# Optimization experiments

Measured on AMD Instinct MI355X. Metric: run time of the kernel, lower is better.

## Reference

```python
import jax, jax.numpy as jnp
import numpy as np

# ---- Cl(3,0) geometric-algebra Cayley table (8 blades: 1,e1,e2,e3,e12,e13,e23,e123) ----
# T[k, i, j] = sign s.t. blade_i * blade_j = sign * blade_k (exactly 8 (i,j) pairs per k).

def _build_cayley():
    masks = [0b000, 0b001, 0b010, 0b100, 0b011, 0b101, 0b110, 0b111]
    T = np.zeros((8, 8, 8), np.float32)
    for i, a in enumerate(masks):
        for j, b in enumerate(masks):
            k = masks.index(a ^ b)
            aa, s = a >> 1, 0
            while aa:
                s += bin(aa & b).count('1')
                aa >>= 1
            T[k, i, j] = -1.0 if (s & 1) else 1.0
    return jnp.asarray(T)

CAYLEY = _build_cayley()
LN_EPS = 1e-5  # torch LayerNorm default


def _layer_norm(x, w, b):
    mu = jnp.mean(x, axis=-1, keepdims=True)
    var = jnp.var(x, axis=-1, keepdims=True)
    return (x - mu) * jax.lax.rsqrt(var + LN_EPS) * w + b


def _expert_forward(x_e, p_in, p_out, iw, gg, w_gate, w_up, w_down, lnw, lnb, out_w, out_b):
    # x_e: (C, D); p_in: (D, ED); per-round params indexed [r]
    C = x_e.shape[0]
    DB = lnw.shape[-1]
    mv = (x_e @ p_in).reshape(C, 8, DB)  # (C, n_blades, d_blade)
    n_rounds = iw.shape[0]
    for r in range(n_rounds):
        w = jax.nn.sigmoid(iw[r]).reshape(8, 8)          # interaction weights w[i,j]
        gate = jax.nn.sigmoid(gg[r])                      # scalar geo gate
        # geo[n,k,d] = sum_{i,j} sign[k,i,j] * w[i,j] * mv[n,i,d] * mv[n,j,d]
        geo = jnp.einsum('kij,ij,nid,njd->nkd', CAYLEY, w, mv, mv)
        mixed = gate * geo + (1.0 - gate) * mv
        flat = _layer_norm(mixed, lnw[r], lnb[r])         # LN over d_blade
        h = jax.nn.silu(flat @ w_gate[r]) * (flat @ w_up[r])  # SwiGLU
        mv = mv + h @ w_down[r]                           # residual
    out = mv.reshape(C, -1) @ p_out                       # (C, D)
    return _layer_norm(out, out_w, out_b)


def setup_inputs() -> dict:
    key = jax.random.key(0)
    ks = jax.random.split(key, 8)
    E, D, NB, DB, R, F = 16, 1024, 8, 64, 2, 256
    ED = NB * DB
    N = 32768
    C = N // E
    std = 0.02
    return {
        'x_sorted': jax.random.normal(ks[0], (N, D), jnp.float32),
        'proj_in': jax.random.normal(ks[1], (E, D, ED), jnp.float32) * std,
        'proj_out': jax.random.normal(ks[2], (E, ED, D), jnp.float32) * std,
        'interaction_weights': jnp.ones((E, R, 64), jnp.float32) * 0.1,
        'geo_gates': jnp.ones((E, R), jnp.float32) * 0.5,
        'ffn_gate': jax.random.normal(ks[3], (E, R, DB, F), jnp.float32) * std,
        'ffn_up': jax.random.normal(ks[4], (E, R, DB, F), jnp.float32) * std,
        'ffn_down': jax.random.normal(ks[5], (E, R, F, DB), jnp.float32) * std,
        'ffn_ln_w': jnp.ones((E, R, DB), jnp.float32),
        'ffn_ln_b': jnp.zeros((E, R, DB), jnp.float32),
        'out_ln_w': jnp.ones((D,), jnp.float32),
        'out_ln_b': jnp.zeros((D,), jnp.float32),
        'expert_offsets': jnp.arange(E, dtype=jnp.int32) * C,
        'expert_counts': jnp.full((E,), C, dtype=jnp.int32),
    }


def reference(x_sorted, proj_in, proj_out, interaction_weights, geo_gates,
              ffn_gate, ffn_up, ffn_down, ffn_ln_w, ffn_ln_b,
              out_ln_w, out_ln_b, expert_offsets, expert_counts):
    E = proj_in.shape[0]
    N, D = x_sorted.shape
    C = N // E  # balanced routing: equal tokens per expert (static shapes)
    idx = expert_offsets[:, None].astype(jnp.int32) + jnp.arange(C, dtype=jnp.int32)[None, :]
    x_b = x_sorted[idx]  # (E, C, D) gather of sorted tokens per expert
    y_b = jax.vmap(_expert_forward,
                   in_axes=(0, 0, 0, 0, 0, 0, 0, 0, 0, 0, None, None))(
        x_b, proj_in, proj_out, interaction_weights, geo_gates,
        ffn_gate, ffn_up, ffn_down, ffn_ln_w, ffn_ln_b, out_ln_w, out_ln_b)
    y = jnp.zeros_like(x_sorted).at[idx.reshape(-1)].set(y_b.reshape(-1, D))
    return y
```

## Files before the change

### kernel.cpp

```cpp
#include <hip/hip_runtime.h>

#define DEV __device__ __forceinline__

typedef __attribute__((ext_vector_type(4))) float f32x4;
typedef __attribute__((ext_vector_type(2))) float f32x2;
typedef __attribute__((ext_vector_type(8))) short bf16x8;


DEV unsigned short f2bf(float f) {
  union { float f; unsigned u; } v; v.f = f;
  unsigned r = v.u + 0x7fffu + ((v.u >> 16) & 1u);
  return (unsigned short)(r >> 16);
}

DEV unsigned pk2bf(float lo, float hi) {
  unsigned r;
  asm("v_cvt_pk_bf16_f32 %0, %1, %2" : "=v"(r) : "v"(lo), "v"(hi));
  return r;
}
DEV unsigned short f2bf1(float v) { return (unsigned short)pk2bf(v, v); }

DEV float bf2f(unsigned short b) {
  union { unsigned u; float f; } v; v.u = ((unsigned)b) << 16; return v.f;
}

DEV float frcp(float x) { return __builtin_amdgcn_rcpf(x); }

DEV void sbar() { asm volatile("s_barrier" ::: "memory"); }
DEV void wait_lgkm0() { asm volatile("s_waitcnt lgkmcnt(0)" ::: "memory"); }
DEV void wait_vm0() { asm volatile("s_waitcnt vmcnt(0)" ::: "memory"); }

DEV void async16(const unsigned short* g, unsigned short* l) {
  __builtin_amdgcn_global_load_lds(
      (__attribute__((address_space(1))) const unsigned int*)g,
      (__attribute__((address_space(3))) unsigned int*)l, 16, 0, 0);
}

DEV long tiled_off(long n, int k, int K) {
  return (n >> 3) * (8L * K) + (long)(((k >> 3) * 64) + ((int)(n & 7)) * 8 + (k & 7));
}

DEV bf16x8 ld_frag(const char* s, int row, int hi) {
  return *(const bf16x8*)(s + ((row >> 3) * 512 + hi * 128 + (row & 7) * 16));
}

__host__ __device__ constexpr int km_(int i) { return i==0?0:i==1?1:i==2?2:i==3?4:i==4?3:i==5?5:i==6?6:7; }
__host__ __device__ constexpr int pc_(int x) { int c = 0; while (x) { c += x & 1; x >>= 1; } return c; }
__host__ __device__ constexpr int KIDX(int i, int j) { return km_(km_(i) ^ km_(j)); }
__host__ __device__ constexpr int CSGN(int i, int j) {
  int a = km_(i), b = km_(j), aa = a >> 1, s = 0;
  while (aa) { s += pc_(aa & b); aa >>= 1; }
  return (s & 1) ? -1 : 1;
}
__host__ __device__ constexpr int PIDX(int i, int j) {
  return 8 * i - (i * (i - 1)) / 2 + (j - i);
}

__global__ __launch_bounds__(64) void geoprep_k(const float* __restrict__ iw,
                                                const float* __restrict__ gg,
                                                float* __restrict__ wcomb) {
  int er = threadIdx.x;
  if (er >= 32) return;
  const float* w = iw + er * 64;
  float gate = frcp(1.f + __expf(-gg[er]));
  float* c = wcomb + er * 40;
  int p = 0;
  for (int i = 0; i < 8; ++i)
    for (int j = i; j < 8; ++j) {
      float v = (float)CSGN(i, j) * frcp(1.f + __expf(-w[i * 8 + j]));
      if (j > i) v += (float)CSGN(j, i) * frcp(1.f + __expf(-w[j * 8 + i]));
      c[p++] = gate * v;
    }
  c[36] = 1.f - gate;
}

template<int TI>
__global__ __launch_bounds__(256) void transpose_k(const float* __restrict__ in,
                                                   unsigned short* __restrict__ out,
                                                   int Rr, int Cc) {
  __shared__ unsigned short tile[32][33];
  const float* ib = in + (long)blockIdx.z * Rr * Cc;
  unsigned short* ob = out + (long)blockIdx.z * Rr * Cc;
  int r0 = blockIdx.y * 32, c0 = blockIdx.x * 32;
  int tr = threadIdx.x >> 5, tc = threadIdx.x & 31;
#pragma unroll
  for (int i = 0; i < 4; ++i) {
    int r = tr + i * 8;
    tile[r][tc] = f2bf(ib[(long)(r0 + r) * Cc + c0 + tc]);
  }
  __syncthreads();
#pragma unroll
  for (int i = 0; i < 4; ++i) {
    int c = tr + i * 8;
    int row = c0 + c;
    int k = r0 + tc;
    if (TI == 0) ob[(long)row * Rr + k] = tile[tc][c];
    else ob[(long)row * Rr + (k ^ ((row & 7) << 3))] = tile[tc][c];
  }
}

__global__ __launch_bounds__(256) void trans_big_k(const float* __restrict__ in,
                                                   unsigned short* __restrict__ out,
                                                   int Rr, int Cc) {
  __shared__ float t[64][64];
  const float* ib = in + (long)blockIdx.z * Rr * Cc;
  unsigned short* ob = out + (long)blockIdx.z * (long)Rr * Cc;
  int k0 = blockIdx.y * 64, n0 = blockIdx.x * 64;
  int tid = threadIdx.x;
#pragma unroll
  for (int p = 0; p < 4; ++p) {
    int idx = p * 256 + tid;
    int kr = idx >> 4, nc = (idx & 15) * 4;
    *(float4*)&t[kr][nc] = *(const float4*)(ib + (long)(k0 + kr) * Cc + n0 + nc);
  }
  __syncthreads();
#pragma unroll
  for (int p = 0; p < 2; ++p) {
    int idx = p * 256 + tid;
    int n = idx & 63, kc = idx >> 6;
    float v[8];
#pragma unroll
    for (int u = 0; u < 8; ++u) v[u] = t[kc * 8 + u][n];
    uint4 o;
    o.x = pk2bf(v[0], v[1]); o.y = pk2bf(v[2], v[3]);
    o.z = pk2bf(v[4], v[5]); o.w = pk2bf(v[6], v[7]);
    *(uint4*)(ob + tiled_off(n0 + n, k0 + kc * 8, Rr)) = o;
  }
}

__global__ __launch_bounds__(512, 1) void gemm_in_k(const float* __restrict__ X,
                                                    const unsigned short* __restrict__ Bw,
                                                    unsigned short* __restrict__ MvB,
                                                    const int* __restrict__ offs) {
  extern __shared__ char smem[];
  int bid = blockIdx.x;
  int wg = (bid & 7) * 32 + (bid >> 3);
  int e = wg >> 4, rem = wg & 15, bm = rem >> 1, bn = rem & 1;
  int tid = threadIdx.x, wid = tid >> 6, lane = tid & 63;
  int wm = (wid >> 2) * 128, wn = (wid & 3) * 64;
  int ri = lane & 15, hi = lane >> 4;
  long rowbase = (long)offs[e] + bm * 256;
  long bw = (long)e * 64 + bn * 32;

  auto STGB = [&](int p) {
    int t = p >> 1, s = p & 1, b = t & 1;
    char* dst = smem + b * 65536 + 32768 + s * 16384;
#pragma unroll
    for (int i = 0; i < 2; ++i) {
      int d = i * 512 + tid;
      async16(Bw + (bw + (d >> 5)) * 8192 +
                  (long)((t * 8 + s * 4 + ((d >> 3) & 3)) * 64 + (d & 7) * 8),
              (unsigned short*)(dst + d * 16));
    }
  };
  auto A_LOAD = [&](int p, float4 ar[2][2]) {
    int t = p >> 1, s = p & 1;
#pragma unroll
    for (int i = 0; i < 2; ++i) {
      int d = i * 512 + tid;
      const float* src = X + (rowbase + ((d >> 5) * 8 + (d & 7))) * 1024 +
                         t * 64 + s * 32 + ((d >> 3) & 3) * 8;
      ar[i][0] = *(const float4*)src;
      ar[i][1] = *(const float4*)(src + 4);
    }
  };
  auto A_WRITE = [&](int p, float4 ar[2][2]) {
    int t = p >> 1, s = p & 1, b = t & 1;
    char* dst = smem + b * 65536 + s * 16384;
#pragma unroll
    for (int i = 0; i < 2; ++i) {
      int d = i * 512 + tid;
      uint4 o;
      o.x = pk2bf(ar[i][0].x, ar[i][0].y);
      o.y = pk2bf(ar[i][0].z, ar[i][0].w);
      o.z = pk2bf(ar[i][1].x, ar[i][1].y);
      o.w = pk2bf(ar[i][1].z, ar[i][1].w);
      *(uint4*)(dst + d * 16) = o;
    }
  };

  f32x4 acc[8][4];
#pragma unroll
  for (int i = 0; i < 8; ++i)
#pragma unroll
    for (int j = 0; j < 4; ++j) acc[i][j] = (f32x4){0.f, 0.f, 0.f, 0.f};

  float4 ar[2][2];
  A_LOAD(0, ar); STGB(0); STGB(1);
  A_WRITE(0, ar);
  A_LOAD(1, ar);
  A_WRITE(1, ar);
  wait_lgkm0();

#pragma unroll 2
  for (int p = 0; p < 32; ++p) {
    int t = p >> 1, s = p & 1, c = t & 1;
    if (p < 30) { A_LOAD(p + 2, ar); STGB(p + 2); }
    if (p < 30) asm volatile("s_waitcnt vmcnt(8)" ::: "memory");
    else if (p == 30) asm volatile("s_waitcnt vmcnt(2)" ::: "memory");
    else asm volatile("s_waitcnt vmcnt(0)" ::: "memory");
    sbar();
    const char* cA = smem + c * 65536 + s * 16384;
    const char* cB = smem + c * 65536 + 32768 + s * 16384;
    bf16x8 a[8], b[4];
#pragma unroll
    for (int i = 0; i < 8; ++i) a[i] = ld_frag(cA, wm + i * 16 + ri, hi);
#pragma unroll
    for (int j = 0; j < 4; ++j) b[j] = ld_frag(cB, wn + j * 16 + ri, hi);
    __builtin_amdgcn_s_setprio(1);
#pragma unroll
    for (int i = 0; i < 8; ++i)
#pragma unroll
      for (int j = 0; j < 4; ++j)
        acc[i][j] = __builtin_amdgcn_mfma_f32_16x16x32_bf16(a[i], b[j], acc[i][j], 0, 0, 0);
    __builtin_amdgcn_s_setprio(0);
    if (p < 30) A_WRITE(p + 2, ar);
    wait_lgkm0();
  }

  unsigned short* Cb = MvB + ((long)e * 2048 + (long)bm * 256) * 512 + bn * 256;
#pragma unroll
  for (int i = 0; i < 8; ++i)
#pragma unroll
    for (int j = 0; j < 4; ++j)
#pragma unroll
      for (int rr = 0; rr < 4; ++rr)
        Cb[(long)(wm + i * 16 + hi * 4 + rr) * 512 + wn + j * 16 + ri] =
            f2bf1(acc[i][j][rr]);
}

__global__ __launch_bounds__(256, 3) void rounds_k(
    const unsigned short* __restrict__ MvB, const unsigned short* __restrict__ WgT,
    const unsigned short* __restrict__ WuT, const unsigned short* __restrict__ WdT,
    const float* __restrict__ wcomb, const float* __restrict__ lnw,
    const float* __restrict__ lnb, unsigned short* __restrict__ Mvb) {
  extern __shared__ char smem[];
  int tid = threadIdx.x, wid = tid >> 6, lane = tid & 63;
  char* sFH = smem + wid * 4096;
  char* sMv = smem + 16384 + wid * 4096;
  char* sW  = smem + 32768;

  int bid = blockIdx.x;
  int wg = (bid & 7) * 256 + (bid >> 3);
  int e = wg >> 7, bx = wg & 127;

  int t4 = lane >> 4, q = lane & 15;
  int ri = lane & 15, hi = lane >> 4;
  int sw = (ri & 7) << 4;

  auto STAGE = [&](int i8) {
    long base = (long)(e * 2 + (i8 >> 3)) * 16384 + (i8 & 7) * 2048;
    char* dst = sW + (i8 & 1) * 8192;
    async16(WgT + base + tid * 8, (unsigned short*)(dst + tid * 16));
    async16(WuT + base + tid * 8, (unsigned short*)(dst + 4096 + tid * 16));
  };
  STAGE(0);

#pragma unroll 1
  for (int r = 0; r < 2; ++r) {
    int er = e * 2 + r;
    const unsigned short* wd = WdT + (long)er * 16384;

    f32x4 mv[8];
    if (r == 0) {
      long base = ((long)e * 2048 + bx * 16 + wid * 4 + t4) * 512 + 4 * q;
      uint2 uv[8];
#pragma unroll
      for (int i = 0; i < 8; ++i)
        uv[i] = *(const uint2*)(MvB + base + i * 64);
#pragma unroll
      for (int i = 0; i < 8; ++i) {
        *(uint2*)(sMv + t4 * 1024 + i * 128 + ((8 * q) ^ (i << 4))) = uv[i];
        mv[i] = (f32x4){bf2f((unsigned short)(uv[i].x & 0xffff)),
                        bf2f((unsigned short)(uv[i].x >> 16)),
                        bf2f((unsigned short)(uv[i].y & 0xffff)),
                        bf2f((unsigned short)(uv[i].y >> 16))};
      }
    } else {
#pragma unroll
      for (int i = 0; i < 8; ++i) {
        uint2 uv = *(const uint2*)(sMv + t4 * 1024 + i * 128 + ((8 * q) ^ (i << 4)));
        mv[i] = (f32x4){bf2f((unsigned short)(uv.x & 0xffff)),
                        bf2f((unsigned short)(uv.x >> 16)),
                        bf2f((unsigned short)(uv.y & 0xffff)),
                        bf2f((unsigned short)(uv.y >> 16))};
      }
    }

    {
      const float* C = wcomb + er * 40;
      f32x4 g[8];
#pragma unroll
      for (int k = 0; k < 8; ++k) g[k] = (f32x4){0.f, 0.f, 0.f, 0.f};
#pragma unroll
      for (int i = 0; i < 8; ++i)
#pragma unroll
        for (int j = i; j < 8; ++j) {
          float cc = C[PIDX(i, j)];
          const int k = KIDX(i, j);
          g[k] += cc * (mv[i] * mv[j]);
        }
      float omg = C[36];
#pragma unroll
      for (int k = 0; k < 8; ++k) g[k] = omg * mv[k] + g[k];
      float4 lw = *(const float4*)(lnw + (long)er * 64 + 4 * q);
      float4 lb = *(const float4*)(lnb + (long)er * 64 + 4 * q);
      f32x4 lwv = (f32x4){lw.x, lw.y, lw.z, lw.w};
      f32x4 lbv = (f32x4){lb.x, lb.y, lb.z, lb.w};
#pragma unroll
      for (int half = 0; half < 2; ++half) {
        f32x2 red[4];
#pragma unroll
        for (int k = 0; k < 4; ++k) {
          f32x4 m = g[half * 4 + k];
          red[k].x = (m.x + m.y) + (m.z + m.w);
          red[k].y = fmaf(m.x, m.x, m.y * m.y) + fmaf(m.z, m.z, m.w * m.w);
        }
#pragma unroll
        for (int off = 8; off >= 1; off >>= 1)
#pragma unroll
          for (int t = 0; t < 4; ++t) {
            f32x2 o;
            o.x = __shfl_xor(red[t].x, off);
            o.y = __shfl_xor(red[t].y, off);
            red[t] += o;
          }
#pragma unroll
        for (int k = 0; k < 4; ++k) {
          int kk = half * 4 + k;
          float mean = red[k].x * (1.f / 64.f);
          float var = red[k].y * (1.f / 64.f) - mean * mean;
          float rs = rsqrtf(var + 1e-5f);
          f32x4 nv = (g[kk] - mean) * rs;
          f32x4 ov = nv * lwv + lbv;
          uint2 pv;
          pv.x = pk2bf(ov.x, ov.y);
          pv.y = pk2bf(ov.z, ov.w);
          int row = t4 * 8 + kk;
          *(uint2*)(sFH + row * 128 + ((8 * q) ^ (kk << 4))) = pv;
        }
      }
    }
    wait_lgkm0();

    bf16x8 bfr[2][2];
#pragma unroll
    for (int tt = 0; tt < 2; ++tt)
#pragma unroll
      for (int kt = 0; kt < 2; ++kt)
        bfr[tt][kt] = *(const bf16x8*)(sFH + (tt * 16 + ri) * 128 + ((kt * 64 + hi * 16) ^ sw));

    f32x4 acc2[4][2];
#pragma unroll
    for (int j = 0; j < 4; ++j)
#pragma unroll
      for (int tt = 0; tt < 2; ++tt) acc2[j][tt] = (f32x4){0.f, 0.f, 0.f, 0.f};

#pragma unroll 1
    for (int q8 = 0; q8 < 8; ++q8) {
      int i8 = r * 8 + q8;
      wait_vm0();
      sbar();
      if (i8 < 15) STAGE(i8 + 1);

      bf16x8 wdf[4];
#pragma unroll
      for (int j = 0; j < 4; ++j)
        wdf[j] = *(const bf16x8*)(wd + (j * 16 + ri) * 256 + q8 * 32 + hi * 8);

      const char* bufW = sW + (i8 & 1) * 8192;

#pragma unroll
      for (int ftl = 0; ftl < 2; ++ftl) {
        const char* bg = bufW + (ftl * 16 + ri) * 128;
        const char* bu = bg + 4096;
        bf16x8 wg0 = *(const bf16x8*)(bg + ((hi * 16) ^ sw));
        bf16x8 wg1 = *(const bf16x8*)(bg + ((64 + hi * 16) ^ sw));
        bf16x8 wu0 = *(const bf16x8*)(bu + ((hi * 16) ^ sw));
        bf16x8 wu1 = *(const bf16x8*)(bu + ((64 + hi * 16) ^ sw));
        f32x4 ag[2], au[2];
#pragma unroll
        for (int tt = 0; tt < 2; ++tt) {
          ag[tt] = (f32x4){0.f, 0.f, 0.f, 0.f};
          au[tt] = (f32x4){0.f, 0.f, 0.f, 0.f};
        }
        __builtin_amdgcn_s_setprio(1);
#pragma unroll
        for (int tt = 0; tt < 2; ++tt) {
          ag[tt] = __builtin_amdgcn_mfma_f32_16x16x32_bf16(wg0, bfr[tt][0], ag[tt], 0, 0, 0);
          au[tt] = __builtin_amdgcn_mfma_f32_16x16x32_bf16(wu0, bfr[tt][0], au[tt], 0, 0, 0);
          ag[tt] = __builtin_amdgcn_mfma_f32_16x16x32_bf16(wg1, bfr[tt][1], ag[tt], 0, 0, 0);
          au[tt] = __builtin_amdgcn_mfma_f32_16x16x32_bf16(wu1, bfr[tt][1], au[tt], 0, 0, 0);
        }
        __builtin_amdgcn_s_setprio(0);
#pragma unroll
        for (int tt = 0; tt < 2; ++tt) {
          float hh[4];
#pragma unroll
          for (int rr = 0; rr < 4; ++rr) {
            float gv = ag[tt][rr], uu = au[tt][rr];
            hh[rr] = gv * uu * frcp(1.f + __expf(-gv));
          }
          uint2 hwv;
          hwv.x = pk2bf(hh[0], hh[1]);
          hwv.y = pk2bf(hh[2], hh[3]);
          *(uint2*)(sFH + (tt * 16 + ri) * 128 + ((ftl * 32 + hi * 8) ^ sw)) = hwv;
        }
      }
      wait_lgkm0();

      bf16x8 hk0 = *(const bf16x8*)(sFH + ri * 128 + ((hi * 16) ^ sw));
      bf16x8 hk1 = *(const bf16x8*)(sFH + (16 + ri) * 128 + ((hi * 16) ^ sw));
      __builtin_amdgcn_s_setprio(1);
#pragma unroll
      for (int j = 0; j < 4; ++j)
        acc2[j][0] = __builtin_amdgcn_mfma_f32_16x16x32_bf16(wdf[j], hk0, acc2[j][0], 0, 0, 0);
#pragma unroll
      for (int j = 0; j < 4; ++j)
        acc2[j][1] = __builtin_amdgcn_mfma_f32_16x16x32_bf16(wdf[j], hk1, acc2[j][1], 0, 0, 0);
      __builtin_amdgcn_s_setprio(0);
    }

    {
#pragma unroll
      for (int tt = 0; tt < 2; ++tt) {
        int tl = tt * 2 + (ri >> 3);
        int kb = ri & 7;
#pragma unroll
        for (int j = 0; j < 4; ++j)
#pragma unroll
          for (int u = 0; u < 2; ++u) {
            int off = (j * 32 + hi * 8 + 4 * u) ^ sw;
            unsigned* p = (unsigned*)(sMv + tl * 1024 + kb * 128 + off);
            unsigned old = *p;
            float v0 = bf2f((unsigned short)(old & 0xffff)) + acc2[j][tt][2 * u];
            float v1 = bf2f((unsigned short)(old >> 16)) + acc2[j][tt][2 * u + 1];
            *p = pk2bf(v0, v1);
          }
      }
    }
    wait_lgkm0();

    if (r == 1) {
      int tt = lane >> 4;
      int idx = lane & 15;
      int bl = idx >> 1;
      int c2 = idx & 1;
      const char* src = sMv + tt * 1024 + bl * 128;
      long row = (long)e * 2048 + bx * 16 + wid * 4 + tt;
      unsigned short* dst = Mvb + row * 512 + bl * 64 + c2 * 32;
#pragma unroll
      for (int h = 0; h < 4; ++h) {
        uint4 v = *(const uint4*)(src + ((c2 * 64 + h * 16) ^ (bl << 4)));
        *(uint4*)(dst + h * 8) = v;
      }
    }
  }
}

__global__ __launch_bounds__(512, 2) void gemm_out_ln_k(
    const unsigned short* __restrict__ Mvb, const unsigned short* __restrict__ Pw,
    float* __restrict__ Out, const float* __restrict__ ow, const float* __restrict__ ob,
    const int* __restrict__ offs) {
  extern __shared__ char smem[];
  int bid = blockIdx.x;
  int wg = (bid & 7) * 64 + (bid >> 3);
  int e = wg >> 5, mb = wg & 31;
  int tid = threadIdx.x, wid = tid >> 6, lane = tid & 63;
  int ri = lane & 15, hi = lane >> 4;
  long bbase = (long)e * 524288;
  long arow0 = (long)e * 2048 + (long)mb * 64;

  auto STAGE = [&](int buf, int kt) {
#pragma unroll
    for (int i = 0; i < 8; ++i) {
      int q = i * 512 + tid;
      int w = q >> 5, c = (q >> 3) & 3, rr = q & 7;
      async16(Pw + bbase + (long)w * 4096 + (kt * 4 + c) * 64 + rr * 8,
              (unsigned short*)(smem + buf * 65536 + q * 16));
    }
    if (tid < 256) {
      int q = tid;
      int w = q >> 5, c = (q >> 3) & 3, rr = q & 7;
      async16(Mvb + (arow0 + w * 8 + rr) * 512 + kt * 32 + c * 8,
              (unsigned short*)(smem + 131072 + buf * 4096 + q * 16));
    }
  };

  f32x4 acc[4][8];
#pragma unroll
  for (int i = 0; i < 4; ++i)
#pragma unroll
    for (int j = 0; j < 8; ++j) acc[i][j] = (f32x4){0.f, 0.f, 0.f, 0.f};

  STAGE(0, 0);
  for (int kt = 0; kt < 16; ++kt) {
    int cur = kt & 1;
    if (kt < 15) {
      STAGE(cur ^ 1, kt + 1);
      asm volatile("s_waitcnt vmcnt(8)" ::: "memory");
    } else {
      asm volatile("s_waitcnt vmcnt(0)" ::: "memory");
    }
    sbar();
    const char* cB = smem + cur * 65536;
    const char* cA = smem + 131072 + cur * 4096;
    bf16x8 a[4], b[8];
#pragma unroll
    for (int i = 0; i < 4; ++i) a[i] = ld_frag(cA, i * 16 + ri, hi);
#pragma unroll
    for (int j = 0; j < 8; ++j) b[j] = ld_frag(cB, wid * 128 + j * 16 + ri, hi);
    __builtin_amdgcn_s_setprio(1);
#pragma unroll
    for (int i = 0; i < 4; ++i)
#pragma unroll
      for (int j = 0; j < 8; ++j)
        acc[i][j] = __builtin_amdgcn_mfma_f32_16x16x32_bf16(a[i], b[j], acc[i][j], 0, 0, 0);
    __builtin_amdgcn_s_setprio(0);
    sbar();
  }

  float* rsum = (float*)(smem + 139264);
  float* rsq  = (float*)(smem + 141312);
  float* mexp = (float*)(smem + 143360);
  float* rstd = (float*)(smem + 143616);
  int hi4 = hi * 4;
#pragma unroll
  for (int i = 0; i < 4; ++i)
#pragma unroll
    for (int rr = 0; rr < 4; ++rr) {
      float s = 0.f, qv = 0.f;
#pragma unroll
      for (int j = 0; j < 8; ++j) { float v = acc[i][j][rr]; s += v; qv += v * v; }
#pragma unroll
      for (int off = 1; off < 16; off <<= 1) {
        s += __shfl_xor(s, off);
        qv += __shfl_xor(qv, off);
      }
      if (ri == 0) {
        int row = i * 16 + hi4 + rr;
        rsum[row * 8 + wid] = s;
        rsq[row * 8 + wid] = qv;
      }
    }
  __syncthreads();
  if (tid < 64) {
    float S = 0.f, Q = 0.f;
#pragma unroll
    for (int w = 0; w < 8; ++w) { S += rsum[tid * 8 + w]; Q += rsq[tid * 8 + w]; }
    float mean = S * (1.f / 1024.f);
    float var = Q * (1.f / 1024.f) - mean * mean;
    mexp[tid] = mean;
    rstd[tid] = rsqrtf(var + 1e-5f);
  }
  __syncthreads();
  long r0 = (long)offs[e] + (long)mb * 64;
  float owv[8], obv[8];
#pragma unroll
  for (int j = 0; j < 8; ++j) {
    int col = wid * 128 + j * 16 + ri;
    owv[j] = ow[col];
    obv[j] = ob[col];
  }
#pragma unroll
  for (int i = 0; i < 4; ++i)
#pragma unroll
    for (int rr = 0; rr < 4; ++rr) {
      int row = i * 16 + hi4 + rr;
      float mu = mexp[row], rs = rstd[row];
#pragma unroll
      for (int j = 0; j < 8; ++j) {
        int col = wid * 128 + j * 16 + ri;
        Out[(r0 + row) * 1024 + col] = (acc[i][j][rr] - mu) * rs * owv[j] + obv[j];
      }
    }
}

extern "C" void kernel_launch(void* const* d_in, const int* in_sizes, int n_in,
                              void* d_out, int out_size, void* d_ws, size_t ws_size,
                              hipStream_t stream) {
  const float* x    = (const float*)d_in[0];
  const float* pin  = (const float*)d_in[1];
  const float* pout = (const float*)d_in[2];
  const float* iw   = (const float*)d_in[3];
  const float* gg   = (const float*)d_in[4];
  const float* fg   = (const float*)d_in[5];
  const float* fu   = (const float*)d_in[6];
  const float* fd   = (const float*)d_in[7];
  const float* lnw  = (const float*)d_in[8];
  const float* lnb  = (const float*)d_in[9];
  const float* ow   = (const float*)d_in[10];
  const float* ob   = (const float*)d_in[11];
  const int* offs   = (const int*)d_in[12];

  char* ws = (char*)d_ws;
  unsigned short* mvB  = (unsigned short*)(ws + 0L);
  unsigned short* mvb  = (unsigned short*)(ws + 33554432L);
  unsigned short* pinT = (unsigned short*)(ws + 67108864L);
  unsigned short* poutT= (unsigned short*)(ws + 83886080L);
  unsigned short* wgT  = (unsigned short*)(ws + 100663296L);
  unsigned short* wuT  = (unsigned short*)(ws + 102760448L);
  unsigned short* wdT  = (unsigned short*)(ws + 104857600L);
  float* wcomb         = (float*)(ws + 106954752L);

  trans_big_k<<<dim3(8, 16, 16), dim3(256), 0, stream>>>(pin, pinT, 1024, 512);
  trans_big_k<<<dim3(16, 8, 16), dim3(256), 0, stream>>>(pout, poutT, 512, 1024);
  transpose_k<1><<<dim3(8, 2, 32), dim3(256), 0, stream>>>(fg, wgT, 64, 256);
  transpose_k<1><<<dim3(8, 2, 32), dim3(256), 0, stream>>>(fu, wuT, 64, 256);
  transpose_k<0><<<dim3(2, 8, 32), dim3(256), 0, stream>>>(fd, wdT, 256, 64);
  geoprep_k<<<dim3(1), dim3(64), 0, stream>>>(iw, gg, wcomb);

  gemm_in_k<<<dim3(256), dim3(512), 131072, stream>>>(x, pinT, mvB, offs);

  rounds_k<<<dim3(2048), dim3(256), 49152, stream>>>(
      mvB, wgT, wuT, wdT, wcomb, lnw, lnb, mvb);

  gemm_out_ln_k<<<dim3(512), dim3(512), 143872, stream>>>(
      mvb, poutT, (float*)d_out, ow, ob, offs);
}
```

Measured before the change: 274.4 us.

## Double tokens per wave in rounds kernel to amortize weight fragment loads

```diff
diff --git a/kernel.cpp b/kernel.cpp
--- a/kernel.cpp
+++ b/kernel.cpp
@@ -229,22 +229,22 @@
             f2bf1(acc[i][j][rr]);
 }
 
-__global__ __launch_bounds__(256, 3) void rounds_k(
+__global__ __launch_bounds__(256, 2) void rounds_k(
     const unsigned short* __restrict__ MvB, const unsigned short* __restrict__ WgT,
     const unsigned short* __restrict__ WuT, const unsigned short* __restrict__ WdT,
     const float* __restrict__ wcomb, const float* __restrict__ lnw,
     const float* __restrict__ lnb, unsigned short* __restrict__ Mvb) {
   extern __shared__ char smem[];
   int tid = threadIdx.x, wid = tid >> 6, lane = tid & 63;
-  char* sFH = smem + wid * 4096;
-  char* sMv = smem + 16384 + wid * 4096;
-  char* sW  = smem + 32768;
+  char* sFH = smem + wid * 8192;
+  char* sMv = smem + 32768 + wid * 8192;
+  char* sW  = smem + 65536;
 
   int bid = blockIdx.x;
-  int wg = (bid & 7) * 256 + (bid >> 3);
-  int e = wg >> 7, bx = wg & 127;
-
-  int t4 = lane >> 4, q = lane & 15;
+  int wg = (bid & 7) * 128 + (bid >> 3);
+  int e = wg >> 6, bx = wg & 63;
+
+  int t8 = lane >> 3, q = lane & 7;
   int ri = lane & 15, hi = lane >> 4;
   int sw = (ri & 7) << 4;
 
@@ -261,63 +261,81 @@
     int er = e * 2 + r;
     const unsigned short* wd = WdT + (long)er * 16384;
 
-    f32x4 mv[8];
+    f32x4 mv[2][8];
     if (r == 0) {
-      long base = ((long)e * 2048 + bx * 16 + wid * 4 + t4) * 512 + 4 * q;
-      uint2 uv[8];
+      long base = ((long)e * 2048 + bx * 32 + wid * 8 + t8) * 512 + 8 * q;
+      uint4 uv[8];
 #pragma unroll
       for (int i = 0; i < 8; ++i)
-        uv[i] = *(const uint2*)(MvB + base + i * 64);
+        uv[i] = *(const uint4*)(MvB + base + i * 64);
 #pragma unroll
       for (int i = 0; i < 8; ++i) {
-        *(uint2*)(sMv + t4 * 1024 + i * 128 + ((8 * q) ^ (i << 4))) = uv[i];
-        mv[i] = (f32x4){bf2f((unsigned short)(uv[i].x & 0xffff)),
-                        bf2f((unsigned short)(uv[i].x >> 16)),
-                        bf2f((unsigned short)(uv[i].y & 0xffff)),
-                        bf2f((unsigned short)(uv[i].y >> 16))};
+        *(uint4*)(sMv + t8 * 1024 + i * 128 + ((16 * q) ^ (i << 4))) = uv[i];
+        mv[0][i] = (f32x4){bf2f((unsigned short)(uv[i].x & 0xffff)),
+                           bf2f((unsigned short)(uv[i].x >> 16)),
+                           bf2f((unsigned short)(uv[i].y & 0xffff)),
+                           bf2f((unsigned short)(uv[i].y >> 16))};
+        mv[1][i] = (f32x4){bf2f((unsigned short)(uv[i].z & 0xffff)),
+                           bf2f((unsigned short)(uv[i].z >> 16)),
+                           bf2f((unsigned short)(uv[i].w & 0xffff)),
+                           bf2f((unsigned short)(uv[i].w >> 16))};
       }
     } else {
 #pragma unroll
       for (int i = 0; i < 8; ++i) {
-        uint2 uv = *(const uint2*)(sMv + t4 * 1024 + i * 128 + ((8 * q) ^ (i << 4)));
-        mv[i] = (f32x4){bf2f((unsigned short)(uv.x & 0xffff)),
-                        bf2f((unsigned short)(uv.x >> 16)),
-                        bf2f((unsigned short)(uv.y & 0xffff)),
-                        bf2f((unsigned short)(uv.y >> 16))};
+        uint4 uv = *(const uint4*)(sMv + t8 * 1024 + i * 128 + ((16 * q) ^ (i << 4)));
+        mv[0][i] = (f32x4){bf2f((unsigned short)(uv.x & 0xffff)),
+                           bf2f((unsigned short)(uv.x >> 16)),
+                           bf2f((unsigned short)(uv.y & 0xffff)),
+                           bf2f((unsigned short)(uv.y >> 16))};
+        mv[1][i] = (f32x4){bf2f((unsigned short)(uv.z & 0xffff)),
+                           bf2f((unsigned short)(uv.z >> 16)),
+                           bf2f((unsigned short)(uv.w & 0xffff)),
+                           bf2f((unsigned short)(uv.w >> 16))};
       }
     }
 
     {
       const float* C = wcomb + er * 40;
-      f32x4 g[8];
-#pragma unroll
-      for (int k = 0; k < 8; ++k) g[k] = (f32x4){0.f, 0.f, 0.f, 0.f};
+      f32x4 g[2][8];
+#pragma unroll
+      for (int hf = 0; hf < 2; ++hf)
+#pragma unroll
+        for (int k = 0; k < 8; ++k) g[hf][k] = (f32x4){0.f, 0.f, 0.f, 0.f};
 #pragma unroll
       for (int i = 0; i < 8; ++i)
 #pragma unroll
         for (int j = i; j < 8; ++j) {
           float cc = C[PIDX(i, j)];
           const int k = KIDX(i, j);
-          g[k] += cc * (mv[i] * mv[j]);
+          g[0][k] += cc * (mv[0][i] * mv[0][j]);
+          g[1][k] += cc * (mv[1][i] * mv[1][j]);
         }
       float omg = C[36];
 #pragma unroll
-      for (int k = 0; k < 8; ++k) g[k] = omg * mv[k] + g[k];
-      float4 lw = *(const float4*)(lnw + (long)er * 64 + 4 * q);
-      float4 lb = *(const float4*)(lnb + (long)er * 64 + 4 * q);
-      f32x4 lwv = (f32x4){lw.x, lw.y, lw.z, lw.w};
-      f32x4 lbv = (f32x4){lb.x, lb.y, lb.z, lb.w};
-#pragma unroll
-      for (int half = 0; half < 2; ++half) {
+      for (int hf = 0; hf < 2; ++hf)
+#pragma unroll
+        for (int k = 0; k < 8; ++k) g[hf][k] = omg * mv[hf][k] + g[hf][k];
+      float4 lwa = *(const float4*)(lnw + (long)er * 64 + 8 * q);
+      float4 lwb = *(const float4*)(lnw + (long)er * 64 + 8 * q + 4);
+      float4 lba = *(const float4*)(lnb + (long)er * 64 + 8 * q);
+      float4 lbb = *(const float4*)(lnb + (long)er * 64 + 8 * q + 4);
+      f32x4 lwvA = (f32x4){lwa.x, lwa.y, lwa.z, lwa.w};
+      f32x4 lwvB = (f32x4){lwb.x, lwb.y, lwb.z, lwb.w};
+      f32x4 lbvA = (f32x4){lba.x, lba.y, lba.z, lba.w};
+      f32x4 lbvB = (f32x4){lbb.x, lbb.y, lbb.z, lbb.w};
+#pragma unroll
+      for (int bh = 0; bh < 2; ++bh) {
         f32x2 red[4];
 #pragma unroll
         for (int k = 0; k < 4; ++k) {
-          f32x4 m = g[half * 4 + k];
-          red[k].x = (m.x + m.y) + (m.z + m.w);
-          red[k].y = fmaf(m.x, m.x, m.y * m.y) + fmaf(m.z, m.z, m.w * m.w);
+          f32x4 a = g[0][bh * 4 + k], b = g[1][bh * 4 + k];
+          red[k].x = ((a.x + a.y) + (a.z + a.w)) + ((b.x + b.y) + (b.z + b.w));
+          red[k].y = (fmaf(a.x, a.x, a.y * a.y) + fmaf(a.z, a.z, a.w * a.w)) +
+                     (fmaf(b.x, b.x, b.y * b.y) + fmaf(b.z, b.z, b.w * b.w));
         }
 #pragma unroll
-        for (int off = 8; off >= 1; off >>= 1)
+        for (int off = 4; off >= 1; off >>= 1)
 #pragma unroll
           for (int t = 0; t < 4; ++t) {
             f32x2 o;
@@ -327,34 +345,36 @@
           }
 #pragma unroll
         for (int k = 0; k < 4; ++k) {
-          int kk = half * 4 + k;
+          int kk = bh * 4 + k;
           float mean = red[k].x * (1.f / 64.f);
           float var = red[k].y * (1.f / 64.f) - mean * mean;
           float rs = rsqrtf(var + 1e-5f);
-          f32x4 nv = (g[kk] - mean) * rs;
-          f32x4 ov = nv * lwv + lbv;
-          uint2 pv;
-          pv.x = pk2bf(ov.x, ov.y);
-          pv.y = pk2bf(ov.z, ov.w);
-          int row = t4 * 8 + kk;
-          *(uint2*)(sFH + row * 128 + ((8 * q) ^ (kk << 4))) = pv;
+          f32x4 ovA = ((g[0][kk] - mean) * rs) * lwvA + lbvA;
+          f32x4 ovB = ((g[1][kk] - mean) * rs) * lwvB + lbvB;
+          uint4 pv;
+          pv.x = pk2bf(ovA.x, ovA.y);
+          pv.y = pk2bf(ovA.z, ovA.w);
+          pv.z = pk2bf(ovB.x, ovB.y);
+          pv.w = pk2bf(ovB.z, ovB.w);
+          int row = t8 * 8 + kk;
+          *(uint4*)(sFH + row * 128 + ((16 * q) ^ (kk << 4))) = pv;
         }
       }
     }
     wait_lgkm0();
 
-    bf16x8 bfr[2][2];
-#pragma unroll
-    for (int tt = 0; tt < 2; ++tt)
+    bf16x8 bfr[4][2];
+#pragma unroll
+    for (int tt = 0; tt < 4; ++tt)
 #pragma unroll
       for (int kt = 0; kt < 2; ++kt)
         bfr[tt][kt] = *(const bf16x8*)(sFH + (tt * 16 + ri) * 128 + ((kt * 64 + hi * 16) ^ sw));
 
-    f32x4 acc2[4][2];
+    f32x4 acc2[4][4];
 #pragma unroll
     for (int j = 0; j < 4; ++j)
 #pragma unroll
-      for (int tt = 0; tt < 2; ++tt) acc2[j][tt] = (f32x4){0.f, 0.f, 0.f, 0.f};
+      for (int tt = 0; tt < 4; ++tt) acc2[j][tt] = (f32x4){0.f, 0.f, 0.f, 0.f};
 
 #pragma unroll 1
     for (int q8 = 0; q8 < 8; ++q8) {
@@ -378,15 +398,15 @@
         bf16x8 wg1 = *(const bf16x8*)(bg + ((64 + hi * 16) ^ sw));
         bf16x8 wu0 = *(const bf16x8*)(bu + ((hi * 16) ^ sw));
         bf16x8 wu1 = *(const bf16x8*)(bu + ((64 + hi * 16) ^ sw));
-        f32x4 ag[2], au[2];
-#pragma unroll
-        for (int tt = 0; tt < 2; ++tt) {
+        f32x4 ag[4], au[4];
+#pragma unroll
+        for (int tt = 0; tt < 4; ++tt) {
           ag[tt] = (f32x4){0.f, 0.f, 0.f, 0.f};
           au[tt] = (f32x4){0.f, 0.f, 0.f, 0.f};
         }
         __builtin_amdgcn_s_setprio(1);
 #pragma unroll
-        for (int tt = 0; tt < 2; ++tt) {
+        for (int tt = 0; tt < 4; ++tt) {
           ag[tt] = __builtin_amdgcn_mfma_f32_16x16x32_bf16(wg0, bfr[tt][0], ag[tt], 0, 0, 0);
           au[tt] = __builtin_amdgcn_mfma_f32_16x16x32_bf16(wu0, bfr[tt][0], au[tt], 0, 0, 0);
           ag[tt] = __builtin_amdgcn_mfma_f32_16x16x32_bf16(wg1, bfr[tt][1], ag[tt], 0, 0, 0);
@@ -394,7 +414,7 @@
         }
         __builtin_amdgcn_s_setprio(0);
 #pragma unroll
-        for (int tt = 0; tt < 2; ++tt) {
+        for (int tt = 0; tt < 4; ++tt) {
           float hh[4];
 #pragma unroll
           for (int rr = 0; rr < 4; ++rr) {
@@ -409,21 +429,22 @@
       }
       wait_lgkm0();
 
-      bf16x8 hk0 = *(const bf16x8*)(sFH + ri * 128 + ((hi * 16) ^ sw));
-      bf16x8 hk1 = *(const bf16x8*)(sFH + (16 + ri) * 128 + ((hi * 16) ^ sw));
+      bf16x8 hk[4];
+#pragma unroll
+      for (int tt = 0; tt < 4; ++tt)
+        hk[tt] = *(const bf16x8*)(sFH + (tt * 16 + ri) * 128 + ((hi * 16) ^ sw));
       __builtin_amdgcn_s_setprio(1);
 #pragma unroll
       for (int j = 0; j < 4; ++j)
-        acc2[j][0] = __builtin_amdgcn_mfma_f32_16x16x32_bf16(wdf[j], hk0, acc2[j][0], 0, 0, 0);
-#pragma unroll
-      for (int j = 0; j < 4; ++j)
-        acc2[j][1] = __builtin_amdgcn_mfma_f32_16x16x32_bf16(wdf[j], hk1, acc2[j][1], 0, 0, 0);
+#pragma unroll
+        for (int tt = 0; tt < 4; ++tt)
+          acc2[j][tt] = __builtin_amdgcn_mfma_f32_16x16x32_bf16(wdf[j], hk[tt], acc2[j][tt], 0, 0, 0);
       __builtin_amdgcn_s_setprio(0);
     }
 
     {
 #pragma unroll
-      for (int tt = 0; tt < 2; ++tt) {
+      for (int tt = 0; tt < 4; ++tt) {
         int tl = tt * 2 + (ri >> 3);
         int kb = ri & 7;
 #pragma unroll
@@ -442,17 +463,12 @@
     wait_lgkm0();
 
     if (r == 1) {
-      int tt = lane >> 4;
-      int idx = lane & 15;
-      int bl = idx >> 1;
-      int c2 = idx & 1;
-      const char* src = sMv + tt * 1024 + bl * 128;
-      long row = (long)e * 2048 + bx * 16 + wid * 4 + tt;
-      unsigned short* dst = Mvb + row * 512 + bl * 64 + c2 * 32;
-#pragma unroll
-      for (int h = 0; h < 4; ++h) {
-        uint4 v = *(const uint4*)(src + ((c2 * 64 + h * 16) ^ (bl << 4)));
-        *(uint4*)(dst + h * 8) = v;
+      int bl = lane >> 3, qq = lane & 7;
+      long sbase = ((long)e * 2048 + bx * 32 + wid * 8) * 512;
+#pragma unroll
+      for (int h = 0; h < 8; ++h) {
+        uint4 v = *(const uint4*)(sMv + h * 1024 + bl * 128 + ((16 * qq) ^ (bl << 4)));
+        *(uint4*)(Mvb + sbase + h * 512 + lane * 8) = v;
       }
     }
   }
@@ -612,7 +628,7 @@
 
   gemm_in_k<<<dim3(256), dim3(512), 131072, stream>>>(x, pinT, mvB, offs);
 
-  rounds_k<<<dim3(2048), dim3(256), 49152, stream>>>(
+  rounds_k<<<dim3(1024), dim3(256), 81920, stream>>>(
       mvB, wgT, wuT, wdT, wcomb, lnw, lnb, mvb);
 
   gemm_out_ln_k<<<dim3(512), dim3(512), 143872, stream>>>(
```

After: 264.4 us. 3.6% less time.
